# Kernel optimization log

Hardware: AMD Instinct MI355X
Metric: run time of the kernel (lower is better)

## Reference

```python
import jax, jax.numpy as jnp
import numpy as np

N_NODES = 100000
N_EDGES = 600000
N_GRAPHS = 64
BN_EPS = 1e-5


def setup_inputs() -> dict:
    key = jax.random.key(0)
    ks = jax.random.split(key, 32)
    inp = {
        "x": jax.random.normal(ks[0], (N_NODES, 128), dtype=jnp.float32),
        "edge_index": jax.random.randint(ks[1], (2, N_EDGES), 0, N_NODES, dtype=jnp.int64),
        "batch": jnp.sort(jax.random.randint(ks[2], (N_NODES,), 0, N_GRAPHS, dtype=jnp.int64)),
    }
    dims = [(128, 64, 64), (64, 64, 64), (64, 64, 96)]  # (in, hid, out) per GIN layer
    ki = 3
    for i, (d_in, d_hid, d_out) in enumerate(dims):
        inp[f"l{i}_w1"] = jax.random.normal(ks[ki], (d_in, d_hid), dtype=jnp.float32) * 0.05; ki += 1
        inp[f"l{i}_b1"] = jnp.zeros((d_hid,), dtype=jnp.float32)
        inp[f"l{i}_w2"] = jax.random.normal(ks[ki], (d_hid, d_out), dtype=jnp.float32) * 0.05; ki += 1
        inp[f"l{i}_b2"] = jnp.zeros((d_out,), dtype=jnp.float32)
        inp[f"bn{i}_g"] = jax.random.uniform(ks[ki], (d_out,), minval=0.5, maxval=1.5, dtype=jnp.float32); ki += 1
        inp[f"bn{i}_b"] = jax.random.normal(ks[ki], (d_out,), dtype=jnp.float32) * 0.05; ki += 1
        inp[f"bn{i}_m"] = jax.random.normal(ks[ki], (d_out,), dtype=jnp.float32) * 0.05; ki += 1
        inp[f"bn{i}_v"] = jax.random.uniform(ks[ki], (d_out,), minval=0.5, maxval=1.5, dtype=jnp.float32); ki += 1
    return inp


def _gin_layer(x, src, dst, w1, b1, w2, b2, g, bb, m, v):
    # GINConv (eps=0): h_i = MLP(x_i + sum_{j: j->i} x_j)
    aggr = jax.ops.segment_sum(x[src], dst, num_segments=N_NODES)
    h = x + aggr
    h = jax.nn.relu(h @ w1 + b1) @ w2 + b2
    # eval-mode BatchNorm1d + ReLU
    h = (h - m) * jax.lax.rsqrt(v + BN_EPS) * g + bb
    return jax.nn.relu(h)


def reference(x, edge_index, batch,
              l0_w1, l0_b1, l0_w2, l0_b2, bn0_g, bn0_b, bn0_m, bn0_v,
              l1_w1, l1_b1, l1_w2, l1_b2, bn1_g, bn1_b, bn1_m, bn1_v,
              l2_w1, l2_b1, l2_w2, l2_b2, bn2_g, bn2_b, bn2_m, bn2_v):
    src, dst = edge_index[0], edge_index[1]
    h = _gin_layer(x, src, dst, l0_w1, l0_b1, l0_w2, l0_b2, bn0_g, bn0_b, bn0_m, bn0_v)
    h = _gin_layer(h, src, dst, l1_w1, l1_b1, l1_w2, l1_b2, bn1_g, bn1_b, bn1_m, bn1_v)
    h = _gin_layer(h, src, dst, l2_w1, l2_b1, l2_w2, l2_b2, bn2_g, bn2_b, bn2_m, bn2_v)
    # global mean pool over graphs
    sums = jax.ops.segment_sum(h, batch, num_segments=N_GRAPHS)
    counts = jax.ops.segment_sum(jnp.ones((h.shape[0],), dtype=h.dtype), batch, num_segments=N_GRAPHS)
    return sums / jnp.maximum(counts, 1.0)[:, None]
```

## Files before the change

### kernel.cpp

```cpp
#include <hip/hip_runtime.h>

#define N_NODES 100000
#define N_GRAPHS 64
#define N_EDGES 600000
#define BN_EPS 1e-5f

__global__ void deg_hist_kernel(const int* __restrict__ dst,
                                int* __restrict__ deg, int n_edges) {
    int e = blockIdx.x * blockDim.x + threadIdx.x;
    if (e < n_edges) atomicAdd(&deg[dst[e]], 1);
}

__global__ void scan1_kernel(const int* __restrict__ deg, int* __restrict__ excl,
                             int* __restrict__ partials, int n) {
    __shared__ int s[1024];
    int i = blockIdx.x * 1024 + threadIdx.x;
    int v = (i < n) ? deg[i] : 0;
    s[threadIdx.x] = v;
    __syncthreads();
    for (int off = 1; off < 1024; off <<= 1) {
        int t = (threadIdx.x >= (unsigned)off) ? s[threadIdx.x - off] : 0;
        __syncthreads();
        s[threadIdx.x] += t;
        __syncthreads();
    }
    if (i < n) excl[i] = s[threadIdx.x] - v;
    if (threadIdx.x == 1023) partials[blockIdx.x] = s[1023];
}

__global__ void scan2_kernel(int* partials, int nb) {
    __shared__ int s[128];
    int t = threadIdx.x;
    int v = (t < nb) ? partials[t] : 0;
    s[t] = v;
    __syncthreads();
    for (int off = 1; off < 128; off <<= 1) {
        int u = (t >= off) ? s[t - off] : 0;
        __syncthreads();
        s[t] += u;
        __syncthreads();
    }
    if (t < nb) partials[t] = s[t] - v;
}

__global__ void scan3_kernel(int* __restrict__ rowptr, const int* __restrict__ partials,
                             int n, int total) {
    int i = blockIdx.x * blockDim.x + threadIdx.x;
    if (i < n) rowptr[i] += partials[i >> 10];
    else if (i == n) rowptr[n] = total;
}

__global__ void csr_fill_kernel(const int* __restrict__ src, const int* __restrict__ dst,
                                const int* __restrict__ rowptr, int* __restrict__ cursor,
                                int* __restrict__ eids, int n_edges) {
    int e = blockIdx.x * blockDim.x + threadIdx.x;
    if (e >= n_edges) return;
    int t = dst[e];
    int pos = rowptr[t] + atomicAdd(&cursor[t], 1);
    eids[pos] = src[e];
}

__global__ void graph_bounds_kernel(const int* __restrict__ batch,
                                    int* __restrict__ gstart, int n_nodes) {
    int n = blockIdx.x * blockDim.x + threadIdx.x;
    if (n >= n_nodes) return;
    if (n == 0) {
        for (int g = 0; g <= batch[0]; ++g) gstart[g] = 0;
    } else {
        int b0 = batch[n - 1], b1 = batch[n];
        for (int g = b0 + 1; g <= b1; ++g) gstart[g] = n;
    }
    if (n == n_nodes - 1) {
        for (int g = batch[n] + 1; g <= N_GRAPHS; ++g) gstart[g] = n_nodes;
    }
}

__global__ void prep_kernel(const float* __restrict__ w1, const float* __restrict__ w2,
                            const float* __restrict__ b2, const float* __restrict__ g,
                            const float* __restrict__ bb, const float* __restrict__ m,
                            const float* __restrict__ v,
                            float* __restrict__ w1T, float* __restrict__ w2sT,
                            float* __restrict__ bias2, int DIN, int DOUT) {
    int i = blockIdx.x * blockDim.x + threadIdx.x;
    if (i < 64 * DIN) {
        int j = i / DIN, k = i % DIN;
        w1T[i] = w1[k * 64 + j];
    }
    int i2 = i - 64 * DIN;
    if (i2 >= 0 && i2 < DOUT * 64) {
        int c = i2 / 64, j = i2 % 64;
        float s = g[c] * rsqrtf(v[c] + BN_EPS);
        w2sT[i2] = w2[j * DOUT + c] * s;
    }
    int i3 = i2 - DOUT * 64;
    if (i3 >= 0 && i3 < DOUT) {
        float s = g[i3] * rsqrtf(v[i3] + BN_EPS);
        bias2[i3] = (b2[i3] - m[i3]) * s + bb[i3];
    }
}

__global__ __launch_bounds__(256)
void pre_gemm_kernel(const float* __restrict__ x, const float* __restrict__ w1T,
                     float* __restrict__ y, int n_nodes) {
    constexpr int SA = 132;
    __shared__ float xT[64 * SA];
    __shared__ float w1s[64 * 128];
    const int tid = threadIdx.x;
    const long base = (long)blockIdx.x * 64;

    for (int i4 = tid; i4 < 16 * 128; i4 += 256) {
        int row = i4 >> 5, k4 = i4 & 31;
        long r = base + row;
        if (r >= n_nodes) r = n_nodes - 1;
        *(float4*)&xT[row * SA + k4 * 4] = ((const float4*)x)[r * 32 + k4];
    }
    const float4* gw1 = (const float4*)w1T;
    for (int i4 = tid; i4 < 16 * 128; i4 += 256) {
        int row = i4 >> 5, k4 = i4 & 31;
        *(float4*)&w1s[row * 128 + ((k4 ^ ((row >> 2) & 7)) << 2)] = gw1[i4];
    }
    __syncthreads();

    const int jg = tid & 15, ng = tid >> 4, xw = jg & 7;
    const float* ap = &xT[(ng * 4) * SA];
    const float* wp = &w1s[(jg * 4) * 128];
    float acc[4][4] = {};
    #pragma unroll 4
    for (int k4 = 0; k4 < 32; ++k4) {
        const int ko = (k4 ^ xw) << 2;
        float4 w0 = *(const float4*)&wp[0 * 128 + ko];
        float4 w1v = *(const float4*)&wp[1 * 128 + ko];
        float4 w2v = *(const float4*)&wp[2 * 128 + ko];
        float4 w3v = *(const float4*)&wp[3 * 128 + ko];
        #pragma unroll
        for (int i = 0; i < 4; ++i) {
            float4 a = *(const float4*)&ap[i * SA + k4 * 4];
            acc[i][0] = fmaf(a.x, w0.x, fmaf(a.y, w0.y, fmaf(a.z, w0.z, fmaf(a.w, w0.w, acc[i][0]))));
            acc[i][1] = fmaf(a.x, w1v.x, fmaf(a.y, w1v.y, fmaf(a.z, w1v.z, fmaf(a.w, w1v.w, acc[i][1]))));
            acc[i][2] = fmaf(a.x, w2v.x, fmaf(a.y, w2v.y, fmaf(a.z, w2v.z, fmaf(a.w, w2v.w, acc[i][2]))));
            acc[i][3] = fmaf(a.x, w3v.x, fmaf(a.y, w3v.y, fmaf(a.z, w3v.z, fmaf(a.w, w3v.w, acc[i][3]))));
        }
    }
    #pragma unroll
    for (int i = 0; i < 4; ++i) {
        long n = base + ng * 4 + i;
        if (n < n_nodes) {
            float4 v = {acc[i][0], acc[i][1], acc[i][2], acc[i][3]};
            *(float4*)(y + n * 64 + jg * 4) = v;
        }
    }
}

__global__ __launch_bounds__(256)
void gather64_kernel(const float* __restrict__ y, const int* __restrict__ rowptr,
                     const int* __restrict__ eids, float* __restrict__ g, int n_nodes) {
    int node = blockIdx.x * 16 + (threadIdx.x >> 4);
    if (node >= n_nodes) return;
    int f4 = threadIdx.x & 15;
    const float4* yv = (const float4*)y;
    float4 acc = yv[(long)node * 16 + f4];
    int b = rowptr[node], e = rowptr[node + 1];
    int i = b;
    for (; i + 3 < e; i += 4) {
        int s0 = eids[i], s1 = eids[i + 1], s2 = eids[i + 2], s3 = eids[i + 3];
        float4 r0 = yv[(long)s0 * 16 + f4];
        float4 r1 = yv[(long)s1 * 16 + f4];
        float4 r2 = yv[(long)s2 * 16 + f4];
        float4 r3 = yv[(long)s3 * 16 + f4];
        acc.x += (r0.x + r1.x) + (r2.x + r3.x);
        acc.y += (r0.y + r1.y) + (r2.y + r3.y);
        acc.z += (r0.z + r1.z) + (r2.z + r3.z);
        acc.w += (r0.w + r1.w) + (r2.w + r3.w);
    }
    for (; i < e; ++i) {
        int s = eids[i];
        float4 r = yv[(long)s * 16 + f4];
        acc.x += r.x; acc.y += r.y; acc.z += r.z; acc.w += r.w;
    }
    ((float4*)g)[(long)node * 16 + f4] = acc;
}

__global__ __launch_bounds__(256)
void fused_mid_kernel(const float* __restrict__ g, const float* __restrict__ b1,
                      const float* __restrict__ w2sT, const float* __restrict__ bias2,
                      const float* __restrict__ w1nT, float* __restrict__ ynext,
                      int n_nodes) {
    constexpr int SS = 68;
    __shared__ float sT[64 * SS];
    __shared__ float w2s[64 * 64];
    __shared__ float w1n[64 * 64];
    const int tid = threadIdx.x;
    const long base = (long)blockIdx.x * 64;

    const float4* gg = (const float4*)(g + base * 64);
    for (int i4 = tid; i4 < 16 * 64; i4 += 256) {
        int row = i4 >> 4, k4 = i4 & 15;
        float4 v = gg[i4];
        float4 b = *(const float4*)&b1[k4 * 4];
        v.x = fmaxf(v.x + b.x, 0.0f);
        v.y = fmaxf(v.y + b.y, 0.0f);
        v.z = fmaxf(v.z + b.z, 0.0f);
        v.w = fmaxf(v.w + b.w, 0.0f);
        *(float4*)&sT[row * SS + k4 * 4] = v;
    }
    const float4* gw2 = (const float4*)w2sT;
    for (int i4 = tid; i4 < 16 * 64; i4 += 256) {
        int row = i4 >> 4, k4 = i4 & 15;
        *(float4*)&w2s[row * 64 + ((k4 ^ ((row >> 2) & 7)) << 2)] = gw2[i4];
    }
    const float4* gw1n = (const float4*)w1nT;
    for (int i4 = tid; i4 < 16 * 64; i4 += 256) {
        int row = i4 >> 4, k4 = i4 & 15;
        *(float4*)&w1n[row * 64 + ((k4 ^ ((row >> 2) & 7)) << 2)] = gw1n[i4];
    }
    __syncthreads();

    const int jg = tid & 15, ng = tid >> 4, xw = jg & 7;

    float h[4][4];
    {
        const float* ap = &sT[(ng * 4) * SS];
        const float* wp = &w2s[(jg * 4) * 64];
        float acc[4][4] = {};
        #pragma unroll 4
        for (int k4 = 0; k4 < 16; ++k4) {
            const int ko = (k4 ^ xw) << 2;
            float4 w0 = *(const float4*)&wp[0 * 64 + ko];
            float4 w1v = *(const float4*)&wp[1 * 64 + ko];
            float4 w2v = *(const float4*)&wp[2 * 64 + ko];
            float4 w3v = *(const float4*)&wp[3 * 64 + ko];
            #pragma unroll
            for (int i = 0; i < 4; ++i) {
                float4 a = *(const float4*)&ap[i * SS + k4 * 4];
                acc[i][0] = fmaf(a.x, w0.x, fmaf(a.y, w0.y, fmaf(a.z, w0.z, fmaf(a.w, w0.w, acc[i][0]))));
                acc[i][1] = fmaf(a.x, w1v.x, fmaf(a.y, w1v.y, fmaf(a.z, w1v.z, fmaf(a.w, w1v.w, acc[i][1]))));
                acc[i][2] = fmaf(a.x, w2v.x, fmaf(a.y, w2v.y, fmaf(a.z, w2v.z, fmaf(a.w, w2v.w, acc[i][2]))));
                acc[i][3] = fmaf(a.x, w3v.x, fmaf(a.y, w3v.y, fmaf(a.z, w3v.z, fmaf(a.w, w3v.w, acc[i][3]))));
            }
        }
        float4 bv = *(const float4*)&bias2[jg * 4];
        #pragma unroll
        for (int i = 0; i < 4; ++i) {
            h[i][0] = fmaxf(acc[i][0] + bv.x, 0.0f);
            h[i][1] = fmaxf(acc[i][1] + bv.y, 0.0f);
            h[i][2] = fmaxf(acc[i][2] + bv.z, 0.0f);
            h[i][3] = fmaxf(acc[i][3] + bv.w, 0.0f);
        }
    }
    __syncthreads();
    #pragma unroll
    for (int i = 0; i < 4; ++i) {
        float4 hv = {h[i][0], h[i][1], h[i][2], h[i][3]};
        *(float4*)&sT[(ng * 4 + i) * SS + jg * 4] = hv;
    }
    __syncthreads();

    {
        const float* ap = &sT[(ng * 4) * SS];
        const float* wp = &w1n[(jg * 4) * 64];
        float acc[4][4] = {};
        #pragma unroll 4
        for (int k4 = 0; k4 < 16; ++k4) {
            const int ko = (k4 ^ xw) << 2;
            float4 w0 = *(const float4*)&wp[0 * 64 + ko];
            float4 w1v = *(const float4*)&wp[1 * 64 + ko];
            float4 w2v = *(const float4*)&wp[2 * 64 + ko];
            float4 w3v = *(const float4*)&wp[3 * 64 + ko];
            #pragma unroll
            for (int i = 0; i < 4; ++i) {
                float4 a = *(const float4*)&ap[i * SS + k4 * 4];
                acc[i][0] = fmaf(a.x, w0.x, fmaf(a.y, w0.y, fmaf(a.z, w0.z, fmaf(a.w, w0.w, acc[i][0]))));
                acc[i][1] = fmaf(a.x, w1v.x, fmaf(a.y, w1v.y, fmaf(a.z, w1v.z, fmaf(a.w, w1v.w, acc[i][1]))));
                acc[i][2] = fmaf(a.x, w2v.x, fmaf(a.y, w2v.y, fmaf(a.z, w2v.z, fmaf(a.w, w2v.w, acc[i][2]))));
                acc[i][3] = fmaf(a.x, w3v.x, fmaf(a.y, w3v.y, fmaf(a.z, w3v.z, fmaf(a.w, w3v.w, acc[i][3]))));
            }
        }
        #pragma unroll
        for (int i = 0; i < 4; ++i) {
            long n = base + ng * 4 + i;
            if (n < n_nodes) {
                float4 v = {acc[i][0], acc[i][1], acc[i][2], acc[i][3]};
                *(float4*)(ynext + n * 64 + jg * 4) = v;
            }
        }
    }
}

__global__ __launch_bounds__(256)
void fused_final_kernel(const float* __restrict__ g, const float* __restrict__ b1,
                        const float* __restrict__ w2sT, const float* __restrict__ bias2,
                        float* __restrict__ out, int n_nodes) {
    constexpr int SS = 68;
    constexpr int CPT = 6;
    __shared__ float sT[64 * SS];
    __shared__ float w2s[96 * 64];
    const int tid = threadIdx.x;
    const long base = (long)blockIdx.x * 64;

    const float4* gg = (const float4*)(g + base * 64);
    for (int i4 = tid; i4 < 16 * 64; i4 += 256) {
        int row = i4 >> 4, k4 = i4 & 15;
        float4 v = gg[i4];
        float4 b = *(const float4*)&b1[k4 * 4];
        v.x = fmaxf(v.x + b.x, 0.0f);
        v.y = fmaxf(v.y + b.y, 0.0f);
        v.z = fmaxf(v.z + b.z, 0.0f);
        v.w = fmaxf(v.w + b.w, 0.0f);
        *(float4*)&sT[row * SS + k4 * 4] = v;
    }
    const float4* gw2 = (const float4*)w2sT;
    for (int i4 = tid; i4 < 96 * 16; i4 += 256) {
        int row = i4 >> 4, k4 = i4 & 15;
        *(float4*)&w2s[row * 64 + ((k4 ^ ((row / CPT) & 7)) << 2)] = gw2[i4];
    }
    __syncthreads();

    const int cg = tid & 15, ng = tid >> 4, xw = cg & 7;
    const float* hp = &sT[(ng * 4) * SS];
    const float* wp = &w2s[(cg * CPT) * 64];
    float acc[4][CPT] = {};
    #pragma unroll 4
    for (int k4 = 0; k4 < 16; ++k4) {
        const int ko = (k4 ^ xw) << 2;
        float4 wv[CPT];
        #pragma unroll
        for (int c = 0; c < CPT; ++c) wv[c] = *(const float4*)&wp[c * 64 + ko];
        #pragma unroll
        for (int i = 0; i < 4; ++i) {
            float4 h = *(const float4*)&hp[i * SS + k4 * 4];
            #pragma unroll
            for (int c = 0; c < CPT; ++c)
                acc[i][c] = fmaf(h.x, wv[c].x, fmaf(h.y, wv[c].y, fmaf(h.z, wv[c].z, fmaf(h.w, wv[c].w, acc[i][c]))));
        }
    }
    float bv[CPT];
    #pragma unroll
    for (int c = 0; c < CPT; ++c) bv[c] = bias2[cg * CPT + c];
    #pragma unroll
    for (int i = 0; i < 4; ++i) {
        long n = base + ng * 4 + i;
        if (n < n_nodes) {
            float* op = out + n * 96 + cg * CPT;
            #pragma unroll
            for (int c = 0; c < CPT; ++c) op[c] = fmaxf(acc[i][c] + bv[c], 0.0f);
        }
    }
}

#define POOL_SPLIT 16
__global__ __launch_bounds__(192)
void pool_seg_kernel(const float* __restrict__ h, const int* __restrict__ gstart,
                     float* __restrict__ sums) {
    int g = blockIdx.x >> 4;
    int s = blockIdx.x & 15;
    int lo = gstart[g], hi = gstart[g + 1];
    int len = hi - lo;
    int seg = (len + POOL_SPLIT - 1) / POOL_SPLIT;
    int a = lo + s * seg;
    int b = a + seg; if (b > hi) b = hi;

    int f4 = threadIdx.x % 24;
    int chain = threadIdx.x / 24;
    const float4* hv = (const float4*)h;
    float4 acc = {0.0f, 0.0f, 0.0f, 0.0f};
    for (int n = a + chain; n < b; n += 8) {
        float4 v = hv[(long)n * 24 + f4];
        acc.x += v.x; acc.y += v.y; acc.z += v.z; acc.w += v.w;
    }
    __shared__ float4 red[8][24];
    red[chain][f4] = acc;
    __syncthreads();
    if (threadIdx.x < 24) {
        float4 t = red[0][threadIdx.x];
        #pragma unroll
        for (int c = 1; c < 8; ++c) {
            float4 r = red[c][threadIdx.x];
            t.x += r.x; t.y += r.y; t.z += r.z; t.w += r.w;
        }
        float* sp = &sums[g * 96 + threadIdx.x * 4];
        atomicAdd(sp + 0, t.x);
        atomicAdd(sp + 1, t.y);
        atomicAdd(sp + 2, t.z);
        atomicAdd(sp + 3, t.w);
    }
}

__global__ void finalize_kernel(const float* __restrict__ sums,
                                const int* __restrict__ gstart,
                                float* __restrict__ out) {
    int i = blockIdx.x * blockDim.x + threadIdx.x;
    if (i >= N_GRAPHS * 96) return;
    int g = i / 96;
    float cnt = (float)(gstart[g + 1] - gstart[g]);
    out[i] = sums[i] / fmaxf(cnt, 1.0f);
}

static inline int cdiv_l(long a, int b) { return (int)((a + b - 1) / b); }

extern "C" void kernel_launch(void* const* d_in, const int* in_sizes, int n_in,
                              void* d_out, int out_size, void* d_ws, size_t ws_size,
                              hipStream_t stream) {
    const float* x     = (const float*)d_in[0];
    const int*   ei    = (const int*)d_in[1];
    const int*   src   = ei;
    const int*   dst   = ei + N_EDGES;
    const int*   batch = (const int*)d_in[2];

    const float* P[3][8];
    int p = 3;
    for (int l = 0; l < 3; ++l)
        for (int q = 0; q < 8; ++q)
            P[l][q] = (const float*)d_in[p++];

    const long NP = N_NODES + 64;
    float* ws   = (float*)d_ws;
    float* yT   = ws;
    float* gB   = yT + NP * 64;
    float* h2   = gB + NP * 64;
    float* q    = h2 + NP * 96;
    float* w1T[3], *w2sT[3], *bias2[3];
    for (int l = 0; l < 3; ++l) {
        w1T[l] = q;   q += 64 * 128;
        w2sT[l] = q;  q += 96 * 64;
        bias2[l] = q; q += 96;
    }
    float* sums   = q;
    int* gstart   = (int*)(sums + N_GRAPHS * 96);
    int* deg      = gstart + 72;
    int* cursor   = deg + N_NODES;
    int* partials = cursor + N_NODES;
    int* rowptr   = partials + 128;
    int* eids     = rowptr + (N_NODES + 1);

    const int B = 256;
    const int DIN[3]  = {128, 64, 64};
    const int DOUT[3] = {64, 64, 96};

    for (int l = 0; l < 3; ++l) {
        int tot = 64 * DIN[l] + 64 * DOUT[l] + DOUT[l];
        prep_kernel<<<cdiv_l(tot, B), B, 0, stream>>>(
            P[l][0], P[l][2], P[l][3], P[l][4], P[l][5], P[l][6], P[l][7],
            w1T[l], w2sT[l], bias2[l], DIN[l], DOUT[l]);
    }

    hipMemsetAsync(deg, 0, (size_t)(2 * N_NODES + 128) * sizeof(int), stream);
    deg_hist_kernel<<<cdiv_l(N_EDGES, B), B, 0, stream>>>(dst, deg, N_EDGES);
    int nblk = cdiv_l(N_NODES, 1024);
    scan1_kernel<<<nblk, 1024, 0, stream>>>(deg, rowptr, partials, N_NODES);
    scan2_kernel<<<1, 128, 0, stream>>>(partials, nblk);
    scan3_kernel<<<cdiv_l(N_NODES + 1, B), B, 0, stream>>>(rowptr, partials, N_NODES, N_EDGES);
    csr_fill_kernel<<<cdiv_l(N_EDGES, B), B, 0, stream>>>(src, dst, rowptr, cursor, eids, N_EDGES);
    graph_bounds_kernel<<<cdiv_l(N_NODES, B), B, 0, stream>>>(batch, gstart, N_NODES);

    const int ntiles = cdiv_l(N_NODES, 64);
    const int ngather = cdiv_l(N_NODES, 16);

    pre_gemm_kernel<<<ntiles, 256, 0, stream>>>(x, w1T[0], yT, N_NODES);
    gather64_kernel<<<ngather, 256, 0, stream>>>(yT, rowptr, eids, gB, N_NODES);
    fused_mid_kernel<<<ntiles, 256, 0, stream>>>(
        gB, P[0][1], w2sT[0], bias2[0], w1T[1], yT, N_NODES);
    gather64_kernel<<<ngather, 256, 0, stream>>>(yT, rowptr, eids, gB, N_NODES);
    fused_mid_kernel<<<ntiles, 256, 0, stream>>>(
        gB, P[1][1], w2sT[1], bias2[1], w1T[2], yT, N_NODES);
    gather64_kernel<<<ngather, 256, 0, stream>>>(yT, rowptr, eids, gB, N_NODES);
    fused_final_kernel<<<ntiles, 256, 0, stream>>>(
        gB, P[2][1], w2sT[2], bias2[2], h2, N_NODES);

    hipMemsetAsync(sums, 0, (size_t)(N_GRAPHS * 96) * sizeof(float), stream);
    pool_seg_kernel<<<N_GRAPHS * POOL_SPLIT, 192, 0, stream>>>(h2, gstart, sums);
    finalize_kernel<<<cdiv_l(N_GRAPHS * 96, B), B, 0, stream>>>(
        sums, gstart, (float*)d_out);
}
```

Measured before the change: 432.2 us.

## Read activations directly from global memory and fold bias+ReLU into gather

The GEMM kernels no longer stage the activation tile in shared memory; each thread reads its rows directly from global memory as float4 loads. The b1 bias and ReLU move from the fused MLP kernels into the gather epilogue. The fused_mid kernel reuses a single weight buffer for both GEMMs to cut LDS usage and raise occupancy. The trade-off is that direct global reads are uncoalesced and repeat across the 16 threads sharing a row, so they depend on L1/L2 caching.

New measurement: 433.4 us. No clear change (+0.3%).

```diff
diff --git a/kernel.cpp b/kernel.cpp
--- a/kernel.cpp
+++ b/kernel.cpp
@@ -102,18 +102,10 @@
 __global__ __launch_bounds__(256)
 void pre_gemm_kernel(const float* __restrict__ x, const float* __restrict__ w1T,
                      float* __restrict__ y, int n_nodes) {
-    constexpr int SA = 132;
-    __shared__ float xT[64 * SA];
     __shared__ float w1s[64 * 128];
     const int tid = threadIdx.x;
     const long base = (long)blockIdx.x * 64;
 
-    for (int i4 = tid; i4 < 16 * 128; i4 += 256) {
-        int row = i4 >> 5, k4 = i4 & 31;
-        long r = base + row;
-        if (r >= n_nodes) r = n_nodes - 1;
-        *(float4*)&xT[row * SA + k4 * 4] = ((const float4*)x)[r * 32 + k4];
-    }
     const float4* gw1 = (const float4*)w1T;
     for (int i4 = tid; i4 < 16 * 128; i4 += 256) {
         int row = i4 >> 5, k4 = i4 & 31;
@@ -122,8 +114,14 @@
     __syncthreads();
 
     const int jg = tid & 15, ng = tid >> 4, xw = jg & 7;
-    const float* ap = &xT[(ng * 4) * SA];
     const float* wp = &w1s[(jg * 4) * 128];
+    const float4* xv = (const float4*)x;
+    long r[4];
+    #pragma unroll
+    for (int i = 0; i < 4; ++i) {
+        long rr = base + ng * 4 + i;
+        r[i] = (rr < n_nodes) ? rr : (n_nodes - 1);
+    }
     float acc[4][4] = {};
     #pragma unroll 4
     for (int k4 = 0; k4 < 32; ++k4) {
@@ -134,7 +132,7 @@
         float4 w3v = *(const float4*)&wp[3 * 128 + ko];
         #pragma unroll
         for (int i = 0; i < 4; ++i) {
-            float4 a = *(const float4*)&ap[i * SA + k4 * 4];
+            float4 a = xv[r[i] * 32 + k4];
             acc[i][0] = fmaf(a.x, w0.x, fmaf(a.y, w0.y, fmaf(a.z, w0.z, fmaf(a.w, w0.w, acc[i][0]))));
             acc[i][1] = fmaf(a.x, w1v.x, fmaf(a.y, w1v.y, fmaf(a.z, w1v.z, fmaf(a.w, w1v.w, acc[i][1]))));
             acc[i][2] = fmaf(a.x, w2v.x, fmaf(a.y, w2v.y, fmaf(a.z, w2v.z, fmaf(a.w, w2v.w, acc[i][2]))));
@@ -153,7 +151,8 @@
 
 __global__ __launch_bounds__(256)
 void gather64_kernel(const float* __restrict__ y, const int* __restrict__ rowptr,
-                     const int* __restrict__ eids, float* __restrict__ g, int n_nodes) {
+                     const int* __restrict__ eids, const float* __restrict__ b1,
+                     float* __restrict__ t, int n_nodes) {
     int node = blockIdx.x * 16 + (threadIdx.x >> 4);
     if (node >= n_nodes) return;
     int f4 = threadIdx.x & 15;
@@ -177,50 +176,81 @@
         float4 r = yv[(long)s * 16 + f4];
         acc.x += r.x; acc.y += r.y; acc.z += r.z; acc.w += r.w;
     }
-    ((float4*)g)[(long)node * 16 + f4] = acc;
+    float4 bv = ((const float4*)b1)[f4];
+    float4 o;
+    o.x = fmaxf(acc.x + bv.x, 0.0f);
+    o.y = fmaxf(acc.y + bv.y, 0.0f);
+    o.z = fmaxf(acc.z + bv.z, 0.0f);
+    o.w = fmaxf(acc.w + bv.w, 0.0f);
+    ((float4*)t)[(long)node * 16 + f4] = o;
 }
 
 __global__ __launch_bounds__(256)
-void fused_mid_kernel(const float* __restrict__ g, const float* __restrict__ b1,
-                      const float* __restrict__ w2sT, const float* __restrict__ bias2,
-                      const float* __restrict__ w1nT, float* __restrict__ ynext,
-                      int n_nodes) {
+void fused_mid_kernel(const float* __restrict__ t, const float* __restrict__ w2sT,
+                      const float* __restrict__ bias2, const float* __restrict__ w1nT,
+                      float* __restrict__ ynext, int n_nodes) {
     constexpr int SS = 68;
     __shared__ float sT[64 * SS];
-    __shared__ float w2s[64 * 64];
-    __shared__ float w1n[64 * 64];
+    __shared__ float wbuf[64 * 64];
     const int tid = threadIdx.x;
     const long base = (long)blockIdx.x * 64;
 
-    const float4* gg = (const float4*)(g + base * 64);
-    for (int i4 = tid; i4 < 16 * 64; i4 += 256) {
-        int row = i4 >> 4, k4 = i4 & 15;
-        float4 v = gg[i4];
-        float4 b = *(const float4*)&b1[k4 * 4];
-        v.x = fmaxf(v.x + b.x, 0.0f);
-        v.y = fmaxf(v.y + b.y, 0.0f);
-        v.z = fmaxf(v.z + b.z, 0.0f);
-        v.w = fmaxf(v.w + b.w, 0.0f);
-        *(float4*)&sT[row * SS + k4 * 4] = v;
-    }
     const float4* gw2 = (const float4*)w2sT;
     for (int i4 = tid; i4 < 16 * 64; i4 += 256) {
         int row = i4 >> 4, k4 = i4 & 15;
-        *(float4*)&w2s[row * 64 + ((k4 ^ ((row >> 2) & 7)) << 2)] = gw2[i4];
+        *(float4*)&wbuf[row * 64 + ((k4 ^ ((row >> 2) & 7)) << 2)] = gw2[i4];
+    }
+    __syncthreads();
+
+    const int jg = tid & 15, ng = tid >> 4, xw = jg & 7;
+    const float4* tv = (const float4*)(t + base * 64);
+
+    float h[4][4];
+    {
+        const float* wp = &wbuf[(jg * 4) * 64];
+        float acc[4][4] = {};
+        #pragma unroll 4
+        for (int k4 = 0; k4 < 16; ++k4) {
+            const int ko = (k4 ^ xw) << 2;
+            float4 w0 = *(const float4*)&wp[0 * 64 + ko];
+            float4 w1v = *(const float4*)&wp[1 * 64 + ko];
+            float4 w2v = *(const float4*)&wp[2 * 64 + ko];
+            float4 w3v = *(const float4*)&wp[3 * 64 + ko];
+            #pragma unroll
+            for (int i = 0; i < 4; ++i) {
+                float4 a = tv[(ng * 4 + i) * 16 + k4];
+                acc[i][0] = fmaf(a.x, w0.x, fmaf(a.y, w0.y, fmaf(a.z, w0.z, fmaf(a.w, w0.w, acc[i][0]))));
+                acc[i][1] = fmaf(a.x, w1v.x, fmaf(a.y, w1v.y, fmaf(a.z, w1v.z, fmaf(a.w, w1v.w, acc[i][1]))));
+                acc[i][2] = fmaf(a.x, w2v.x, fmaf(a.y, w2v.y, fmaf(a.z, w2v.z, fmaf(a.w, w2v.w, acc[i][2]))));
+                acc[i][3] = fmaf(a.x, w3v.x, fmaf(a.y, w3v.y, fmaf(a.z, w3v.z, fmaf(a.w, w3v.w, acc[i][3]))));
+            }
+        }
+        float4 bv = *(const float4*)&bias2[jg * 4];
+        #pragma unroll
+        for (int i = 0; i < 4; ++i) {
+            h[i][0] = fmaxf(acc[i][0] + bv.x, 0.0f);
+            h[i][1] = fmaxf(acc[i][1] + bv.y, 0.0f);
+            h[i][2] = fmaxf(acc[i][2] + bv.z, 0.0f);
+            h[i][3] = fmaxf(acc[i][3] + bv.w, 0.0f);
+        }
+    }
+    __syncthreads();
+
+    #pragma unroll
+    for (int i = 0; i < 4; ++i) {
+        float4 hv = {h[i][0], h[i][1], h[i][2], h[i][3]};
+        *(float4*)&sT[(ng * 4 + i) * SS + jg * 4] = hv;
     }
     const float4* gw1n = (const float4*)w1nT;
     for (int i4 = tid; i4 < 16 * 64; i4 += 256) {
         int row = i4 >> 4, k4 = i4 & 15;
-        *(float4*)&w1n[row * 64 + ((k4 ^ ((row >> 2) & 7)) << 2)] = gw1n[i4];
-    }
-    __syncthreads();
-
-    const int jg = tid & 15, ng = tid >> 4, xw = jg & 7;
-
-    float h[4][4];
+        *(float4*)&wbuf[row * 64 + ((k4 ^ ((row >> 2) & 7)) << 2)] = gw1n[i4];
+    }
+    __syncthreads();
+
     {
         const float* ap = &sT[(ng * 4) * SS];
-        const float* wp = &w2s[(jg * 4) * 64];
+        const float* wp = &wbuf[(jg * 4) * 64];
         float acc[4][4] = {};
         #pragma unroll 4
         for (int k4 = 0; k4 < 16; ++k4) {
@@ -238,43 +268,6 @@
                 acc[i][3] = fmaf(a.x, w3v.x, fmaf(a.y, w3v.y, fmaf(a.z, w3v.z, fmaf(a.w, w3v.w, acc[i][3]))));
             }
         }
-        float4 bv = *(const float4*)&bias2[jg * 4];
-        #pragma unroll
-        for (int i = 0; i < 4; ++i) {
-            h[i][0] = fmaxf(acc[i][0] + bv.x, 0.0f);
-            h[i][1] = fmaxf(acc[i][1] + bv.y, 0.0f);
-            h[i][2] = fmaxf(acc[i][2] + bv.z, 0.0f);
-            h[i][3] = fmaxf(acc[i][3] + bv.w, 0.0f);
-        }
-    }
-    __syncthreads();
-    #pragma unroll
-    for (int i = 0; i < 4; ++i) {
-        float4 hv = {h[i][0], h[i][1], h[i][2], h[i][3]};
-        *(float4*)&sT[(ng * 4 + i) * SS + jg * 4] = hv;
-    }
-    __syncthreads();
-
-    {
-        const float* ap = &sT[(ng * 4) * SS];
-        const float* wp = &w1n[(jg * 4) * 64];
-        float acc[4][4] = {};
-        #pragma unroll 4
-        for (int k4 = 0; k4 < 16; ++k4) {
-            const int ko = (k4 ^ xw) << 2;
-            float4 w0 = *(const float4*)&wp[0 * 64 + ko];
-            float4 w1v = *(const float4*)&wp[1 * 64 + ko];
-            float4 w2v = *(const float4*)&wp[2 * 64 + ko];
-            float4 w3v = *(const float4*)&wp[3 * 64 + ko];
-            #pragma unroll
-            for (int i = 0; i < 4; ++i) {
-                float4 a = *(const float4*)&ap[i * SS + k4 * 4];
-                acc[i][0] = fmaf(a.x, w0.x, fmaf(a.y, w0.y, fmaf(a.z, w0.z, fmaf(a.w, w0.w, acc[i][0]))));
-                acc[i][1] = fmaf(a.x, w1v.x, fmaf(a.y, w1v.y, fmaf(a.z, w1v.z, fmaf(a.w, w1v.w, acc[i][1]))));
-                acc[i][2] = fmaf(a.x, w2v.x, fmaf(a.y, w2v.y, fmaf(a.z, w2v.z, fmaf(a.w, w2v.w, acc[i][2]))));
-                acc[i][3] = fmaf(a.x, w3v.x, fmaf(a.y, w3v.y, fmaf(a.z, w3v.z, fmaf(a.w, w3v.w, acc[i][3]))));
-            }
-        }
         #pragma unroll
         for (int i = 0; i < 4; ++i) {
             long n = base + ng * 4 + i;
@@ -287,27 +280,14 @@
 }
 
 __global__ __launch_bounds__(256)
-void fused_final_kernel(const float* __restrict__ g, const float* __restrict__ b1,
-                        const float* __restrict__ w2sT, const float* __restrict__ bias2,
-                        float* __restrict__ out, int n_nodes) {
-    constexpr int SS = 68;
+void fused_final_kernel(const float* __restrict__ t, const float* __restrict__ w2sT,
+                        const float* __restrict__ bias2, float* __restrict__ out,
+                        int n_nodes) {
     constexpr int CPT = 6;
-    __shared__ float sT[64 * SS];
     __shared__ float w2s[96 * 64];
     const int tid = threadIdx.x;
     const long base = (long)blockIdx.x * 64;
 
-    const float4* gg = (const float4*)(g + base * 64);
-    for (int i4 = tid; i4 < 16 * 64; i4 += 256) {
-        int row = i4 >> 4, k4 = i4 & 15;
-        float4 v = gg[i4];
-        float4 b = *(const float4*)&b1[k4 * 4];
-        v.x = fmaxf(v.x + b.x, 0.0f);
-        v.y = fmaxf(v.y + b.y, 0.0f);
-        v.z = fmaxf(v.z + b.z, 0.0f);
-        v.w = fmaxf(v.w + b.w, 0.0f);
-        *(float4*)&sT[row * SS + k4 * 4] = v;
-    }
     const float4* gw2 = (const float4*)w2sT;
     for (int i4 = tid; i4 < 96 * 16; i4 += 256) {
         int row = i4 >> 4, k4 = i4 & 15;
@@ -316,7 +296,7 @@
     __syncthreads();
 
     const int cg = tid & 15, ng = tid >> 4, xw = cg & 7;
-    const float* hp = &sT[(ng * 4) * SS];
+    const float4* tv = (const float4*)(t + base * 64);
     const float* wp = &w2s[(cg * CPT) * 64];
     float acc[4][CPT] = {};
     #pragma unroll 4
@@ -327,7 +307,7 @@
         for (int c = 0; c < CPT; ++c) wv[c] = *(const float4*)&wp[c * 64 + ko];
         #pragma unroll
         for (int i = 0; i < 4; ++i) {
-            float4 h = *(const float4*)&hp[i * SS + k4 * 4];
+            float4 h = tv[(ng * 4 + i) * 16 + k4];
             #pragma unroll
             for (int c = 0; c < CPT; ++c)
                 acc[i][c] = fmaf(h.x, wv[c].x, fmaf(h.y, wv[c].y, fmaf(h.z, wv[c].z, fmaf(h.w, wv[c].w, acc[i][c]))));
@@ -456,15 +436,15 @@
     const int ngather = cdiv_l(N_NODES, 16);
 
     pre_gemm_kernel<<<ntiles, 256, 0, stream>>>(x, w1T[0], yT, N_NODES);
-    gather64_kernel<<<ngather, 256, 0, stream>>>(yT, rowptr, eids, gB, N_NODES);
+    gather64_kernel<<<ngather, 256, 0, stream>>>(yT, rowptr, eids, P[0][1], gB, N_NODES);
     fused_mid_kernel<<<ntiles, 256, 0, stream>>>(
-        gB, P[0][1], w2sT[0], bias2[0], w1T[1], yT, N_NODES);
-    gather64_kernel<<<ngather, 256, 0, stream>>>(yT, rowptr, eids, gB, N_NODES);
+        gB, w2sT[0], bias2[0], w1T[1], yT, N_NODES);
+    gather64_kernel<<<ngather, 256, 0, stream>>>(yT, rowptr, eids, P[1][1], gB, N_NODES);
     fused_mid_kernel<<<ntiles, 256, 0, stream>>>(
-        gB, P[1][1], w2sT[1], bias2[1], w1T[2], yT, N_NODES);
-    gather64_kernel<<<ngather, 256, 0, stream>>>(yT, rowptr, eids, gB, N_NODES);
+        gB, w2sT[1], bias2[1], w1T[2], yT, N_NODES);
+    gather64_kernel<<<ngather, 256, 0, stream>>>(yT, rowptr, eids, P[2][1], gB, N_NODES);
     fused_final_kernel<<<ntiles, 256, 0, stream>>>(
-        gB, P[2][1], w2sT[2], bias2[2], h2, N_NODES);
+        gB, w2sT[2], bias2[2], h2, N_NODES);
 
     hipMemsetAsync(sums, 0, (size_t)(N_GRAPHS * 96) * sizeof(float), stream);
     pool_seg_kernel<<<N_GRAPHS * POOL_SPLIT, 192, 0, stream>>>(h2, gstart, sums);
```
